# Performance work log

Hardware: AMD Instinct MI355X
Metric: run time of the kernel (lower is better)

Reference implementation:

```python
import jax, jax.numpy as jnp
import numpy as np

D_MODEL = 1024
N_HEADS = 16
HEAD_DIM = D_MODEL // N_HEADS
EPS = 1e-6


def setup_inputs() -> dict:
    key = jax.random.key(0)
    ks = jax.random.split(key, 5)
    b, s = 2, 2048
    x = jax.random.normal(ks[0], (b, s, D_MODEL), dtype=jnp.float32)
    scale = 1.0 / np.sqrt(D_MODEL)
    Wq = jax.random.normal(ks[1], (D_MODEL, D_MODEL), dtype=jnp.float32) * scale
    Wk = jax.random.normal(ks[2], (D_MODEL, D_MODEL), dtype=jnp.float32) * scale
    Wv = jax.random.normal(ks[3], (D_MODEL, D_MODEL), dtype=jnp.float32) * scale
    Wo = jax.random.normal(ks[4], (D_MODEL, D_MODEL), dtype=jnp.float32) * scale
    return {"x": x, "Wq": Wq, "Wk": Wk, "Wv": Wv, "Wo": Wo}


def _feature_map(t):
    return jax.nn.relu(t) + EPS


def reference(x, Wq, Wk, Wv, Wo):
    b, s, _ = x.shape
    # nn.Linear applies x @ W.T
    q = (x @ Wq.T).reshape(b, s, N_HEADS, HEAD_DIM)
    k = (x @ Wk.T).reshape(b, s, N_HEADS, HEAD_DIM)
    v = (x @ Wv.T).reshape(b, s, N_HEADS, HEAD_DIM)
    q = _feature_map(q).transpose(0, 2, 1, 3)  # bhsd
    k = _feature_map(k).transpose(0, 2, 1, 3)  # bhsd
    v = v.transpose(0, 2, 1, 3)                # bhsm
    # cumulative KV outer products: (b,h,s,d,m)
    kv = jnp.einsum('bhsd,bhsm->bhsdm', k, v)
    kv_cum = jnp.cumsum(kv, axis=2)
    out = jnp.einsum('bhsd,bhsdm->bhsm', q, kv_cum)
    k_cum = jnp.cumsum(k, axis=2)
    z = 1.0 / (jnp.einsum('bhsd,bhsd->bhs', q, k_cum) + EPS)
    out = out * z[..., None]
    out = out.transpose(0, 2, 1, 3).reshape(b, s, D_MODEL)
    return out @ Wo.T
```

## Files before the change

kernel.cpp:

```cpp
#include <hip/hip_runtime.h>

#define EPSF 1e-6f

typedef short bf16x8_t __attribute__((ext_vector_type(8)));
typedef float f32x4_t __attribute__((ext_vector_type(4)));

__device__ __forceinline__ ushort f2bf(float f) {
  union { float f; uint32_t u; } c; c.f = f;
  return (ushort)((c.u + 0x7FFFu + ((c.u >> 16) & 1u)) >> 16);
}
__device__ __forceinline__ float bf2f(ushort u) {
  union { uint32_t u; float f; } c; c.u = ((uint32_t)u) << 16;
  return c.f;
}

#define SWB(row, kbyte) (((row) << 7) + ((kbyte) ^ (((row) & 7) << 4)))

__global__ __launch_bounds__(256) void cvt5_kernel(
    const float4* __restrict__ x, const float4* __restrict__ wq,
    const float4* __restrict__ wk, const float4* __restrict__ wv,
    const float4* __restrict__ wo,
    ushort4* __restrict__ xb, ushort4* __restrict__ wqb,
    ushort4* __restrict__ wkb, ushort4* __restrict__ wvb,
    ushort4* __restrict__ wob)
{
  const int i = blockIdx.x * 256 + threadIdx.x;
  const float4* src; ushort4* dst; int off;
  if (i < (1 << 20)) { src = x; dst = xb; off = i; }
  else {
    const int j = i - (1 << 20);
    const int r = j >> 18;
    off = j & ((1 << 18) - 1);
    src = (r == 0) ? wq : (r == 1) ? wk : (r == 2) ? wv : wo;
    dst = (r == 0) ? wqb : (r == 1) ? wkb : (r == 2) ? wvb : wob;
  }
  const float4 v = src[off];
  ushort4 o;
  o.x = f2bf(v.x); o.y = f2bf(v.y); o.z = f2bf(v.z); o.w = f2bf(v.w);
  dst[off] = o;
}

template<int BN, int OUT_BF16>
__device__ __forceinline__ void gemm_bt_mfma(
    const ushort* __restrict__ A, const ushort* __restrict__ B,
    void* __restrict__ C, const int K,
    const int N, const int row0, const int col0, const bool relu)
{
  constexpr int NFR = BN / 32;
  __shared__ __align__(16) uint As[2048];
  __shared__ __align__(16) uint Bs[BN * 16];
  const int tid = threadIdx.x;
  const int lane = tid & 63;
  const int wv = tid >> 6;
  const int wr = (wv >> 1) * 64;
  const int wc = (wv & 1) * (BN / 2);

  f32x4_t acc[4][NFR];
#pragma unroll
  for (int m = 0; m < 4; ++m)
#pragma unroll
    for (int n = 0; n < NFR; ++n) acc[m][n] = (f32x4_t){0.f, 0.f, 0.f, 0.f};

  const int fr = lane & 15;
  const int kh = (lane >> 4) * 8;

  for (int k0 = 0; k0 < K; k0 += 32) {
    __syncthreads();
#pragma unroll
    for (int is = 0; is < 2; ++is) {
      const int c = tid + (is << 8);
      const int row = c >> 2, kq = (c & 3) << 3;
      __builtin_amdgcn_global_load_lds(
          (const __attribute__((address_space(1))) void*)(A + (size_t)(row0 + row) * K + k0 + kq),
          (__attribute__((address_space(3))) void*)(As + (c & ~63) * 4), 16, 0, 0);
    }
#pragma unroll
    for (int is = 0; is < BN / 64; ++is) {
      const int c = tid + (is << 8);
      const int row = c >> 2, kq = (c & 3) << 3;
      __builtin_amdgcn_global_load_lds(
          (const __attribute__((address_space(1))) void*)(B + (size_t)(col0 + row) * K + k0 + kq),
          (__attribute__((address_space(3))) void*)(Bs + (c & ~63) * 4), 16, 0, 0);
    }
    __syncthreads();

    bf16x8_t af[4], bfr[NFR];
#pragma unroll
    for (int m = 0; m < 4; ++m)
      af[m] = *(const bf16x8_t*)((const ushort*)As + (size_t)(wr + m * 16 + fr) * 32 + kh);
#pragma unroll
    for (int n = 0; n < NFR; ++n)
      bfr[n] = *(const bf16x8_t*)((const ushort*)Bs + (size_t)(wc + n * 16 + fr) * 32 + kh);
#pragma unroll
    for (int m = 0; m < 4; ++m)
#pragma unroll
      for (int n = 0; n < NFR; ++n)
        acc[m][n] = __builtin_amdgcn_mfma_f32_16x16x32_bf16(
            af[m], bfr[n], acc[m][n], 0, 0, 0);
  }

  const int rq = (lane >> 4) * 4;
#pragma unroll
  for (int m = 0; m < 4; ++m) {
#pragma unroll
    for (int r = 0; r < 4; ++r) {
      const size_t grow = (size_t)(row0 + wr + m * 16 + rq + r);
#pragma unroll
      for (int n = 0; n < NFR; ++n) {
        float val = acc[m][n][r];
        if (relu) val = fmaxf(val, 0.f) + EPSF;
        const size_t gcol = (size_t)(col0 + wc + n * 16 + fr);
        if (OUT_BF16) ((ushort*)C)[grow * N + gcol] = f2bf(val);
        else          ((float*)C)[grow * N + gcol] = val;
      }
    }
  }
}

__global__ __launch_bounds__(256) void qkv_gemm_kernel(
    const ushort* __restrict__ xb,
    const ushort* __restrict__ wqb, const ushort* __restrict__ wkb,
    const ushort* __restrict__ wvb,
    ushort* __restrict__ q, ushort* __restrict__ k, ushort* __restrict__ v)
{
  const int which = blockIdx.y >> 3;
  const int bcol = blockIdx.y & 7;
  const ushort* B = (which == 0) ? wqb : (which == 1) ? wkb : wvb;
  ushort* C = (which == 0) ? q : (which == 1) ? k : v;
  gemm_bt_mfma<128, 1>(xb, B, C, 1024, 1024,
                       blockIdx.x * 128, bcol * 128, which < 2);
}

__global__ __launch_bounds__(256) void out_gemm_kernel(
    const ushort* __restrict__ at, const ushort* __restrict__ wob,
    float* __restrict__ out)
{
  gemm_bt_mfma<64, 0>(at, wob, out, 1024, 1024,
                      blockIdx.x * 128, blockIdx.y * 64, false);
}


__global__ __launch_bounds__(256) void chunk_sums_kernel(
    const ushort* __restrict__ kbuf, const ushort* __restrict__ vbuf,
    float* __restrict__ kvsum, float* __restrict__ ksum)
{
  __shared__ __align__(16) uint Kt[2048];
  __shared__ __align__(16) uint Vt[2048];
  const int chunk = blockIdx.x;
  const int seq = blockIdx.y;
  const int b = seq >> 4, h = seq & 15;
  const int tid = threadIdx.x;
  const size_t base = ((size_t)b * 2048 + chunk * 64) * 1024 + h * 64;

#pragma unroll
  for (int r = 0; r < 2; ++r) {
    const int idx = tid + (r << 8);
    const int j = idx >> 3;
    const int e0 = (idx & 7) << 3;
    const bf16x8_t kv8 = *(const bf16x8_t*)(kbuf + base + (size_t)j * 1024 + e0);
    const bf16x8_t vv8 = *(const bf16x8_t*)(vbuf + base + (size_t)j * 1024 + e0);
#pragma unroll
    for (int t = 0; t < 8; ++t) {
      *(ushort*)((char*)Kt + SWB(e0 + t, j * 2)) = (ushort)kv8[t];
      *(ushort*)((char*)Vt + SWB(e0 + t, j * 2)) = (ushort)vv8[t];
    }
  }
  __syncthreads();

  if (tid < 64) {
    float s = 0.f;
#pragma unroll
    for (int g = 0; g < 8; ++g) {
      const bf16x8_t kr = *(const bf16x8_t*)((char*)Kt + SWB(tid, g * 16));
#pragma unroll
      for (int t = 0; t < 8; ++t) s += bf2f((ushort)kr[t]);
    }
    ksum[((size_t)seq * 32 + chunk) * 64 + tid] = s;
  }

  const int lane = tid & 63;
  const int wv = tid >> 6;
  const int wm = (wv >> 1) * 32;
  const int wd = (wv & 1) * 32;
  const int fr = lane & 15;
  const int khb = (lane >> 4) * 16;

  f32x4_t acc[2][2];
#pragma unroll
  for (int m = 0; m < 2; ++m)
#pragma unroll
    for (int n = 0; n < 2; ++n) acc[m][n] = (f32x4_t){0.f, 0.f, 0.f, 0.f};

#pragma unroll
  for (int kk = 0; kk < 2; ++kk) {
    bf16x8_t av[2], bk[2];
#pragma unroll
    for (int m = 0; m < 2; ++m)
      av[m] = *(const bf16x8_t*)((char*)Vt + SWB(wm + m * 16 + fr, kk * 64 + khb));
#pragma unroll
    for (int n = 0; n < 2; ++n)
      bk[n] = *(const bf16x8_t*)((char*)Kt + SWB(wd + n * 16 + fr, kk * 64 + khb));
#pragma unroll
    for (int m = 0; m < 2; ++m)
#pragma unroll
      for (int n = 0; n < 2; ++n)
        acc[m][n] = __builtin_amdgcn_mfma_f32_16x16x32_bf16(
            av[m], bk[n], acc[m][n], 0, 0, 0);
  }

  const size_t kvbase = ((size_t)seq * 32 + chunk) << 12;
  const int rq = (lane >> 4) * 4;
#pragma unroll
  for (int m = 0; m < 2; ++m)
#pragma unroll
    for (int r = 0; r < 4; ++r) {
      const int mrow = wm + m * 16 + rq + r;
#pragma unroll
      for (int n = 0; n < 2; ++n) {
        const int dcol = wd + n * 16 + fr;
        kvsum[kvbase + (size_t)mrow * 64 + dcol] = acc[m][n][r];
      }
    }
}

__global__ __launch_bounds__(256) void scan_kernel(
    const float* __restrict__ kvsum, ushort* __restrict__ kvsb,
    float* __restrict__ ksum)
{
  const int slice = blockIdx.x & 15;
  const int seq = blockIdx.x >> 4;
  const int e = slice * 256 + threadIdx.x;
  const size_t base = ((size_t)seq << 17) + e;
  float vals[32];
#pragma unroll
  for (int c = 0; c < 32; ++c) vals[c] = kvsum[base + ((size_t)c << 12)];
  float run = 0.f;
#pragma unroll
  for (int c = 0; c < 32; ++c) {
    kvsb[base + ((size_t)c << 12)] = f2bf(run);
    run += vals[c];
  }
  if (slice == 0 && threadIdx.x < 64) {
    const size_t kb = (size_t)seq * 2048 + threadIdx.x;
    float kv2[32];
#pragma unroll
    for (int c = 0; c < 32; ++c) kv2[c] = ksum[kb + (size_t)c * 64];
    float run2 = 0.f;
#pragma unroll
    for (int c = 0; c < 32; ++c) {
      const float t = kv2[c];
      ksum[kb + (size_t)c * 64] = run2;
      run2 += t;
    }
  }
}

__global__ __launch_bounds__(256) void attn_chunk_kernel(
    const ushort* __restrict__ qbuf, const ushort* __restrict__ kbuf,
    const ushort* __restrict__ vbuf, const ushort* __restrict__ kvsb,
    const float* __restrict__ ksum, ushort* __restrict__ attn)
{
  __shared__ __align__(16) uint Qs[2048];
  __shared__ __align__(16) uint Ks[2048];
  __shared__ __align__(16) uint Vt[2048];
  __shared__ __align__(16) uint Pl[2048];
  __shared__ float ksp[64];
  __shared__ float zinv[64];
  const int chunk = blockIdx.x;
  const int seq = blockIdx.y;
  const int b = seq >> 4, h = seq & 15;
  const int tid = threadIdx.x;
  const size_t base = ((size_t)b * 2048 + chunk * 64) * 1024 + h * 64;

#pragma unroll
  for (int r = 0; r < 2; ++r) {
    const int idx = tid + (r << 8);
    const int row = idx >> 3;
    const int e0 = (idx & 7) << 3;
    const int kb = e0 << 1;
    *(bf16x8_t*)((char*)Qs + SWB(row, kb)) =
        *(const bf16x8_t*)(qbuf + base + (size_t)row * 1024 + e0);
    *(bf16x8_t*)((char*)Ks + SWB(row, kb)) =
        *(const bf16x8_t*)(kbuf + base + (size_t)row * 1024 + e0);
    const bf16x8_t vv8 = *(const bf16x8_t*)(vbuf + base + (size_t)row * 1024 + e0);
#pragma unroll
    for (int t = 0; t < 8; ++t)
      *(ushort*)((char*)Vt + SWB(e0 + t, row * 2)) = (ushort)vv8[t];
  }
  if (tid < 64) ksp[tid] = ksum[((size_t)seq * 32 + chunk) * 64 + tid];
  __syncthreads();

  const int lane = tid & 63;
  const int wv = tid >> 6;
  const int wr = (wv >> 1) * 32;
  const int wc = (wv & 1) * 32;
  const int fr = lane & 15;
  const int khb = (lane >> 4) * 16;
  const int rq = (lane >> 4) * 4;

  f32x4_t sf[2][2];
#pragma unroll
  for (int m = 0; m < 2; ++m)
#pragma unroll
    for (int n = 0; n < 2; ++n) sf[m][n] = (f32x4_t){0.f, 0.f, 0.f, 0.f};
#pragma unroll
  for (int kk = 0; kk < 2; ++kk) {
    bf16x8_t aq[2], bk[2];
#pragma unroll
    for (int m = 0; m < 2; ++m)
      aq[m] = *(const bf16x8_t*)((char*)Qs + SWB(wr + m * 16 + fr, kk * 64 + khb));
#pragma unroll
    for (int n = 0; n < 2; ++n)
      bk[n] = *(const bf16x8_t*)((char*)Ks + SWB(wc + n * 16 + fr, kk * 64 + khb));
#pragma unroll
    for (int m = 0; m < 2; ++m)
#pragma unroll
      for (int n = 0; n < 2; ++n)
        sf[m][n] = __builtin_amdgcn_mfma_f32_16x16x32_bf16(
            aq[m], bk[n], sf[m][n], 0, 0, 0);
  }
  __syncthreads();

#pragma unroll
  for (int m = 0; m < 2; ++m)
#pragma unroll
    for (int r = 0; r < 4; ++r) {
      const int i = wr + m * 16 + rq + r;
#pragma unroll
      for (int n = 0; n < 2; ++n) {
        const int j = wc + n * 16 + fr;
        const float pv = (j <= i) ? sf[m][n][r] : 0.f;
        *(ushort*)((char*)Pl + SWB(i, j * 2)) = f2bf(pv);
      }
    }
  const size_t kvbase = ((size_t)seq * 32 + chunk) << 12;
#pragma unroll
  for (int r = 0; r < 2; ++r) {
    const int idx = tid + (r << 8);
    const int mrow = idx >> 3;
    const int d0 = (idx & 7) << 3;
    const bf16x8_t kv8 = *(const bf16x8_t*)(kvsb + kvbase + (size_t)mrow * 64 + d0);
    *(bf16x8_t*)((char*)Ks + SWB(mrow, d0 << 1)) = kv8;
  }
  __syncthreads();

  if (tid < 64) {
    const int i = tid;
    float dsum = 0.f, ssum = 0.f;
#pragma unroll
    for (int g = 0; g < 8; ++g) {
      const bf16x8_t qr = *(const bf16x8_t*)((char*)Qs + SWB(i, g * 16));
      const bf16x8_t pr = *(const bf16x8_t*)((char*)Pl + SWB(i, g * 16));
#pragma unroll
      for (int t = 0; t < 8; ++t) {
        dsum = fmaf(bf2f((ushort)qr[t]), ksp[g * 8 + t], dsum);
        ssum += bf2f((ushort)pr[t]);
      }
    }
    zinv[i] = 1.f / (dsum + ssum + EPSF);
  }

  f32x4_t of[2][2];
#pragma unroll
  for (int m = 0; m < 2; ++m)
#pragma unroll
    for (int n = 0; n < 2; ++n) of[m][n] = (f32x4_t){0.f, 0.f, 0.f, 0.f};
#pragma unroll
  for (int kk = 0; kk < 2; ++kk) {
    bf16x8_t ap[2], bv[2];
#pragma unroll
    for (int m = 0; m < 2; ++m)
      ap[m] = *(const bf16x8_t*)((char*)Pl + SWB(wr + m * 16 + fr, kk * 64 + khb));
#pragma unroll
    for (int n = 0; n < 2; ++n)
      bv[n] = *(const bf16x8_t*)((char*)Vt + SWB(wc + n * 16 + fr, kk * 64 + khb));
#pragma unroll
    for (int m = 0; m < 2; ++m)
#pragma unroll
      for (int n = 0; n < 2; ++n)
        of[m][n] = __builtin_amdgcn_mfma_f32_16x16x32_bf16(
            ap[m], bv[n], of[m][n], 0, 0, 0);
  }
#pragma unroll
  for (int kk = 0; kk < 2; ++kk) {
    bf16x8_t aq[2], bkv[2];
#pragma unroll
    for (int m = 0; m < 2; ++m)
      aq[m] = *(const bf16x8_t*)((char*)Qs + SWB(wr + m * 16 + fr, kk * 64 + khb));
#pragma unroll
    for (int n = 0; n < 2; ++n)
      bkv[n] = *(const bf16x8_t*)((char*)Ks + SWB(wc + n * 16 + fr, kk * 64 + khb));
#pragma unroll
    for (int m = 0; m < 2; ++m)
#pragma unroll
      for (int n = 0; n < 2; ++n)
        of[m][n] = __builtin_amdgcn_mfma_f32_16x16x32_bf16(
            aq[m], bkv[n], of[m][n], 0, 0, 0);
  }
  __syncthreads();

#pragma unroll
  for (int m = 0; m < 2; ++m)
#pragma unroll
    for (int r = 0; r < 4; ++r) {
      const int i = wr + m * 16 + rq + r;
      const float z = zinv[i];
#pragma unroll
      for (int n = 0; n < 2; ++n) {
        const int mcol = wc + n * 16 + fr;
        attn[base + (size_t)i * 1024 + mcol] = f2bf(of[m][n][r] * z);
      }
    }
}

extern "C" void kernel_launch(void* const* d_in, const int* in_sizes, int n_in,
                              void* d_out, int out_size, void* d_ws, size_t ws_size,
                              hipStream_t stream)
{
  (void)in_sizes; (void)n_in; (void)out_size; (void)ws_size;
  const float* x  = (const float*)d_in[0];
  const float* Wq = (const float*)d_in[1];
  const float* Wk = (const float*)d_in[2];
  const float* Wv = (const float*)d_in[3];
  const float* Wo = (const float*)d_in[4];
  float* out = (float*)d_out;

  const size_t NM = (size_t)4096 * 1024;
  ushort* xb  = (ushort*)d_ws;
  ushort* wqb = xb + NM;
  ushort* wkb = wqb + (1 << 20);
  ushort* wvb = wkb + (1 << 20);
  ushort* wob = wvb + (1 << 20);
  ushort* qb  = wob + (1 << 20);
  ushort* kb  = qb + NM;
  ushort* vb  = kb + NM;
  ushort* at  = vb + NM;
  float*  ksm = (float*)(at + NM);
  float*  kvs = ksm + 65536;
  ushort* kvsb = (ushort*)(kvs + NM);

  cvt5_kernel<<<8192, 256, 0, stream>>>(
      (const float4*)x, (const float4*)Wq, (const float4*)Wk,
      (const float4*)Wv, (const float4*)Wo,
      (ushort4*)xb, (ushort4*)wqb, (ushort4*)wkb, (ushort4*)wvb, (ushort4*)wob);
  qkv_gemm_kernel<<<dim3(32, 24), 256, 0, stream>>>(xb, wqb, wkb, wvb, qb, kb, vb);
  chunk_sums_kernel<<<dim3(32, 32), 256, 0, stream>>>(kb, vb, kvs, ksm);
  scan_kernel<<<512, 256, 0, stream>>>(kvs, kvsb, ksm);
  attn_chunk_kernel<<<dim3(32, 32), 256, 0, stream>>>(qb, kb, vb, kvsb, ksm, at);
  out_gemm_kernel<<<dim3(32, 16), 256, 0, stream>>>(at, wob, out);
}
```

Baseline: 158.3 us.

## Double GEMM k-tile to 64 with XOR-swizzled LDS and store chunk sums in bf16

The shared GEMM helper now stages a 64-wide K slice per iteration, using an XOR swizzle on LDS rows, and runs two MFMA sub-steps per barrier pair. This halves the barrier and loop count and is meant to reduce LDS bank conflicts. Separately, the per-chunk KV sums are written as bf16 instead of fp32, which halves the traffic between chunk_sums and scan. That second change rounds the per-chunk partial sums before accumulation, so precision drops slightly.

```diff
diff --git a/kernel.cpp b/kernel.cpp
--- a/kernel.cpp
+++ b/kernel.cpp
@@ -15,6 +15,7 @@
 }
 
 #define SWB(row, kbyte) (((row) << 7) + ((kbyte) ^ (((row) & 7) << 4)))
+#define SWB64(row, kbyte) (((row) << 7) + ((kbyte) ^ (((row) & 7) << 4)))
 
 __global__ __launch_bounds__(256) void cvt5_kernel(
     const float4* __restrict__ x, const float4* __restrict__ wq,
@@ -47,8 +48,8 @@
     const int N, const int row0, const int col0, const bool relu)
 {
   constexpr int NFR = BN / 32;
-  __shared__ __align__(16) uint As[2048];
-  __shared__ __align__(16) uint Bs[BN * 16];
+  __shared__ __align__(16) uint As[4096];
+  __shared__ __align__(16) uint Bs[BN * 32];
   const int tid = threadIdx.x;
   const int lane = tid & 63;
   const int wv = tid >> 6;
@@ -62,41 +63,51 @@
     for (int n = 0; n < NFR; ++n) acc[m][n] = (f32x4_t){0.f, 0.f, 0.f, 0.f};
 
   const int fr = lane & 15;
-  const int kh = (lane >> 4) * 8;
-
-  for (int k0 = 0; k0 < K; k0 += 32) {
+  const int khb = (lane >> 4) << 4;
+
+  int rowA[4], colA[4];
+#pragma unroll
+  for (int is = 0; is < 4; ++is) {
+    const int c = tid + (is << 8);
+    rowA[is] = c >> 3;
+    colA[is] = (((c & 7) ^ ((c >> 3) & 7)) << 3);
+  }
+
+  for (int k0 = 0; k0 < K; k0 += 64) {
     __syncthreads();
 #pragma unroll
-    for (int is = 0; is < 2; ++is) {
+    for (int is = 0; is < 4; ++is) {
       const int c = tid + (is << 8);
-      const int row = c >> 2, kq = (c & 3) << 3;
       __builtin_amdgcn_global_load_lds(
-          (const __attribute__((address_space(1))) void*)(A + (size_t)(row0 + row) * K + k0 + kq),
+          (const __attribute__((address_space(1))) void*)(A + (size_t)(row0 + rowA[is]) * K + k0 + colA[is]),
           (__attribute__((address_space(3))) void*)(As + (c & ~63) * 4), 16, 0, 0);
     }
 #pragma unroll
-    for (int is = 0; is < BN / 64; ++is) {
+    for (int is = 0; is < BN / 32; ++is) {
       const int c = tid + (is << 8);
-      const int row = c >> 2, kq = (c & 3) << 3;
       __builtin_amdgcn_global_load_lds(
-          (const __attribute__((address_space(1))) void*)(B + (size_t)(col0 + row) * K + k0 + kq),
+          (const __attribute__((address_space(1))) void*)(B + (size_t)(col0 + rowA[is]) * K + k0 + colA[is]),
           (__attribute__((address_space(3))) void*)(Bs + (c & ~63) * 4), 16, 0, 0);
     }
     __syncthreads();
 
-    bf16x8_t af[4], bfr[NFR];
-#pragma unroll
-    for (int m = 0; m < 4; ++m)
-      af[m] = *(const bf16x8_t*)((const ushort*)As + (size_t)(wr + m * 16 + fr) * 32 + kh);
-#pragma unroll
-    for (int n = 0; n < NFR; ++n)
-      bfr[n] = *(const bf16x8_t*)((const ushort*)Bs + (size_t)(wc + n * 16 + fr) * 32 + kh);
-#pragma unroll
-    for (int m = 0; m < 4; ++m)
+#pragma unroll
+    for (int kk = 0; kk < 2; ++kk) {
+      const int kb = kk * 64 + khb;
+      bf16x8_t af[4], bfr[NFR];
+#pragma unroll
+      for (int m = 0; m < 4; ++m)
+        af[m] = *(const bf16x8_t*)((const char*)As + SWB64(wr + m * 16 + fr, kb));
 #pragma unroll
       for (int n = 0; n < NFR; ++n)
-        acc[m][n] = __builtin_amdgcn_mfma_f32_16x16x32_bf16(
-            af[m], bfr[n], acc[m][n], 0, 0, 0);
+        bfr[n] = *(const bf16x8_t*)((const char*)Bs + SWB64(wc + n * 16 + fr, kb));
+#pragma unroll
+      for (int m = 0; m < 4; ++m)
+#pragma unroll
+        for (int n = 0; n < NFR; ++n)
+          acc[m][n] = __builtin_amdgcn_mfma_f32_16x16x32_bf16(
+              af[m], bfr[n], acc[m][n], 0, 0, 0);
+    }
   }
 
   const int rq = (lane >> 4) * 4;
@@ -142,7 +153,7 @@
 
 __global__ __launch_bounds__(256) void chunk_sums_kernel(
     const ushort* __restrict__ kbuf, const ushort* __restrict__ vbuf,
-    float* __restrict__ kvsum, float* __restrict__ ksum)
+    ushort* __restrict__ kvs, float* __restrict__ ksum)
 {
   __shared__ __align__(16) uint Kt[2048];
   __shared__ __align__(16) uint Vt[2048];
@@ -218,27 +229,27 @@
 #pragma unroll
       for (int n = 0; n < 2; ++n) {
         const int dcol = wd + n * 16 + fr;
-        kvsum[kvbase + (size_t)mrow * 64 + dcol] = acc[m][n][r];
+        kvs[kvbase + (size_t)mrow * 64 + dcol] = f2bf(acc[m][n][r]);
       }
     }
 }
 
 __global__ __launch_bounds__(256) void scan_kernel(
-    const float* __restrict__ kvsum, ushort* __restrict__ kvsb,
+    const ushort* __restrict__ kvs, ushort* __restrict__ kvsb,
     float* __restrict__ ksum)
 {
   const int slice = blockIdx.x & 15;
   const int seq = blockIdx.x >> 4;
   const int e = slice * 256 + threadIdx.x;
   const size_t base = ((size_t)seq << 17) + e;
-  float vals[32];
-#pragma unroll
-  for (int c = 0; c < 32; ++c) vals[c] = kvsum[base + ((size_t)c << 12)];
+  ushort vals[32];
+#pragma unroll
+  for (int c = 0; c < 32; ++c) vals[c] = kvs[base + ((size_t)c << 12)];
   float run = 0.f;
 #pragma unroll
   for (int c = 0; c < 32; ++c) {
     kvsb[base + ((size_t)c << 12)] = f2bf(run);
-    run += vals[c];
+    run += bf2f(vals[c]);
   }
   if (slice == 0 && threadIdx.x < 64) {
     const size_t kb = (size_t)seq * 2048 + threadIdx.x;
@@ -436,8 +447,8 @@
   ushort* vb  = kb + NM;
   ushort* at  = vb + NM;
   float*  ksm = (float*)(at + NM);
-  float*  kvs = ksm + 65536;
-  ushort* kvsb = (ushort*)(kvs + NM);
+  ushort* kvs = (ushort*)(ksm + 65536);
+  ushort* kvsb = kvs + NM;
 
   cvt5_kernel<<<8192, 256, 0, stream>>>(
       (const float4*)x, (const float4*)Wq, (const float4*)Wk,
```

Measured after the change: 161.5 us. 2.0% more time.
